# Kernel tuning notes

Measured on AMD Instinct MI355X. Metric: run time of the kernel, lower is better.

Reference implementation:

```python
import jax, jax.numpy as jnp
import numpy as np

N = 100000
E = 3200000
D_IN = 128
HEADS = 4
OUT_CH = 64


def setup_inputs() -> dict:
    key = jax.random.key(0)
    kx, ke, kw, kb = jax.random.split(key, 4)
    x = jax.random.normal(kx, (N, D_IN), dtype=jnp.float32)
    edge_index = jax.random.randint(ke, (2, E), 0, N, dtype=jnp.int64)
    # nn.Linear(in_channels, out_channels*heads): weight [out, in] in torch; store as [in, out] for x @ W
    W = jax.random.normal(kw, (D_IN, OUT_CH * HEADS), dtype=jnp.float32) * (1.0 / np.sqrt(D_IN))
    b = jax.random.normal(kb, (OUT_CH * HEADS,), dtype=jnp.float32) * 0.01
    return {"x": x, "edge_index": edge_index, "W": W, "b": b}


def reference(x, edge_index, W, b):
    src, dst = edge_index[0], edge_index[1]
    n = x.shape[0]
    # scatter-add of gathered src features into dst rows (segment sum)
    agg = jax.ops.segment_sum(x[src], dst, num_segments=n)  # [N, D_IN]
    count = jax.ops.segment_sum(jnp.ones((src.shape[0], 1), x.dtype), dst, num_segments=n)  # [N, 1]
    agg = agg / (count + 1e-8)
    # linear on (x + agg); view to [N, heads*out_channels] is a no-op reshape
    return (x + agg) @ W + b
```

## Files before the change

kernel.cpp:

```cpp
#include <hip/hip_runtime.h>

#define N_NODES 100000
#define D_IN 128
#define D_OUT 256
#define NBLK 256
#define NBKT 256
#define BSH  9
#define BNODES 512
#define NBUCKETS ((N_NODES + BNODES - 1) / BNODES)
#define CAP  19456
#define CAPC 12544

typedef __attribute__((ext_vector_type(8))) short short8_t;
typedef __attribute__((ext_vector_type(4))) float f32x4;

__device__ inline unsigned short f2bf_rne(float f) {
    unsigned u = __float_as_uint(f);
    u += 0x7fffu + ((u >> 16) & 1u);
    return (unsigned short)(u >> 16);
}

__global__ __launch_bounds__(256) void convert_kernel(
    const float* __restrict__ x, ushort* __restrict__ xb, int n4)
{
    int i = blockIdx.x * 256 + threadIdx.x;
    if (i < n4) {
        float4 v = ((const float4*)x)[i];
        ushort4 r;
        r.x = f2bf_rne(v.x); r.y = f2bf_rne(v.y);
        r.z = f2bf_rne(v.z); r.w = f2bf_rne(v.w);
        ((ushort4*)xb)[i] = r;
    }
}

__global__ __launch_bounds__(256) void wfrag_kernel(
    const float* __restrict__ W, short8_t* __restrict__ wfrag)
{
    int tid  = blockIdx.x * 256 + threadIdx.x;
    int lane = tid & 63;
    int fi   = tid >> 6;
    int ks   = fi >> 4, nt = fi & 15;
    int k0   = ks * 32 + (lane >> 4) * 8;
    int col  = nt * 16 + (lane & 15);
    short8_t v;
    #pragma unroll
    for (int e = 0; e < 8; e++)
        v[e] = (short)f2bf_rne(W[(size_t)(k0 + e) * D_OUT + col]);
    wfrag[tid] = v;
}

__global__ __launch_bounds__(256) void binA_hist(
    const int* __restrict__ dst, int* __restrict__ blockHist, int E, int chunk)
{
    __shared__ int h[NBKT];
    int b = blockIdx.x, t = threadIdx.x;
    h[t] = 0;
    __syncthreads();
    int e0 = b * chunk, e1 = min(e0 + chunk, E);
    for (int e = e0 + t; e < e1; e += 256)
        atomicAdd(&h[dst[e] >> BSH], 1);
    __syncthreads();
    blockHist[b * NBKT + t] = h[t];
}

__global__ __launch_bounds__(256) void binA_scan(
    int* __restrict__ blockHist, int* __restrict__ bucketTotal)
{
    __shared__ int wsum[4];
    int bucket = blockIdx.x;
    int t = threadIdx.x, lane = t & 63, w = t >> 6;
    int v = blockHist[t * NBKT + bucket];
    int s = v;
    #pragma unroll
    for (int d = 1; d < 64; d <<= 1) {
        int u = __shfl_up(s, d);
        if (lane >= d) s += u;
    }
    if (lane == 63) wsum[w] = s;
    __syncthreads();
    int wo = 0;
    for (int j = 0; j < w; j++) wo += wsum[j];
    blockHist[t * NBKT + bucket] = wo + s - v;
    if (t == 255) {
        int tot = 0;
        for (int j = 0; j < 4; j++) tot += wsum[j];
        bucketTotal[bucket] = tot;
    }
}

__global__ __launch_bounds__(256) void binA_scanbase(
    const int* __restrict__ bucketTotal, int* __restrict__ bucketBase)
{
    __shared__ int wsum[4];
    int t = threadIdx.x, lane = t & 63, w = t >> 6;
    int v = bucketTotal[t];
    int s = v;
    #pragma unroll
    for (int d = 1; d < 64; d <<= 1) {
        int u = __shfl_up(s, d);
        if (lane >= d) s += u;
    }
    if (lane == 63) wsum[w] = s;
    __syncthreads();
    int wo = 0;
    for (int j = 0; j < w; j++) wo += wsum[j];
    bucketBase[t] = wo + s - v;
}

__global__ __launch_bounds__(256) void binA_scatter(
    const int* __restrict__ src, const int* __restrict__ dst,
    const int* __restrict__ blockHist, const int* __restrict__ bucketBase,
    unsigned* __restrict__ pairs, int E, int chunk)
{
    __shared__ unsigned stage[CAPC];
    __shared__ int cnt[NBKT];
    __shared__ int lofs[NBKT];
    __shared__ int rankl[NBKT];
    __shared__ int gcur[NBKT];
    __shared__ int wsum[4];

    int b = blockIdx.x, t = threadIdx.x, lane = t & 63, w = t >> 6;
    int e0 = b * chunk, e1 = min(e0 + chunk, E);

    gcur[t] = bucketBase[t] + blockHist[b * NBKT + t];
    __syncthreads();

    for (int c0 = e0; c0 < e1; c0 += CAPC) {
        int c1 = c0 + CAPC; if (c1 > e1) c1 = e1;

        cnt[t] = 0;
        __syncthreads();

        for (int e = c0 + t; e < c1; e += 256)
            atomicAdd(&cnt[dst[e] >> BSH], 1);
        __syncthreads();

        {
            int v = cnt[t];
            int s = v;
            #pragma unroll
            for (int d = 1; d < 64; d <<= 1) {
                int u = __shfl_up(s, d);
                if (lane >= d) s += u;
            }
            if (lane == 63) wsum[w] = s;
            __syncthreads();
            int wo = 0;
            for (int j = 0; j < w; j++) wo += wsum[j];
            int excl = wo + s - v;
            lofs[t]  = excl;
            rankl[t] = excl;
        }
        __syncthreads();

        for (int e = c0 + t; e < c1; e += 256) {
            int d = dst[e];
            int bin = d >> BSH;
            int pos = atomicAdd(&rankl[bin], 1);
            stage[pos] = ((unsigned)(d & (BNODES - 1)) << 17) | (unsigned)src[e];
        }
        __syncthreads();

        for (int bin = w; bin < NBKT; bin += 4) {
            int lo = lofs[bin], c = cnt[bin], g = gcur[bin];
            for (int i = lane; i < c; i += 64)
                pairs[g + i] = stage[lo + i];
        }
        __syncthreads();

        gcur[t] += cnt[t];
        __syncthreads();
    }
}

__global__ __launch_bounds__(256) void binB_sort(
    unsigned* __restrict__ pairs, const int* __restrict__ bucketBase,
    int* __restrict__ offs_g, int* __restrict__ deg_g)
{
    __shared__ unsigned stage[CAP];
    __shared__ int hist[BNODES];
    __shared__ int rank[BNODES];
    __shared__ int wsum[4];

    int b = blockIdx.x, t = threadIdx.x, lane = t & 63, w = t >> 6;
    int e0 = bucketBase[b], e1 = bucketBase[b + 1];
    int cnt = e1 - e0;
    if (cnt > CAP) cnt = CAP;

    hist[t] = 0; hist[t + 256] = 0;
    __syncthreads();

    for (int i = t; i < cnt; i += 256) {
        unsigned p = pairs[e0 + i];
        stage[i] = p;
        atomicAdd(&hist[p >> 17], 1);
    }
    __syncthreads();

    int a0 = hist[t * 2], a1 = hist[t * 2 + 1];
    int v = a0 + a1;
    int s = v;
    #pragma unroll
    for (int d = 1; d < 64; d <<= 1) {
        int u = __shfl_up(s, d);
        if (lane >= d) s += u;
    }
    if (lane == 63) wsum[w] = s;
    __syncthreads();
    int wo = 0;
    for (int j = 0; j < w; j++) wo += wsum[j];
    int excl = wo + s - v;

    rank[t * 2]     = excl;
    rank[t * 2 + 1] = excl + a0;
    int node = (b << BSH) + t * 2;
    if (node < N_NODES) {
        offs_g[node] = e0 + excl;
        deg_g[node]  = a0;
    }
    if (node + 1 < N_NODES) {
        offs_g[node + 1] = e0 + excl + a0;
        deg_g[node + 1]  = a1;
    }
    __syncthreads();

    for (int i = t; i < cnt; i += 256) {
        unsigned p = stage[i];
        int pos = atomicAdd(&rank[p >> 17], 1);
        pairs[e0 + pos] = p & 0x1FFFFu;
    }
}

template <bool USE_BF16>
__global__ __launch_bounds__(256) void fused_kernel(
    const float* __restrict__ x,
    const ushort* __restrict__ xb,
    const int* __restrict__ offs,
    const int* __restrict__ deg,
    const int* __restrict__ sorted_src,
    const short8_t* __restrict__ wfrag,
    const float* __restrict__ b,
    float* __restrict__ out)
{
    __shared__ __align__(16) ushort shb[16 * D_IN];

    int n0   = blockIdx.x * 16;
    int t    = threadIdx.x;
    int lane = t & 63;
    int w    = t >> 6;

    for (int nn = 0; nn < 4; nn++) {
        int nl = w * 4 + nn;
        int n  = n0 + nl;
        int start = offs[n];
        int d     = deg[n];
        float accx = 0.0f, accy = 0.0f;
        for (int base = 0; base < d; base += 64) {
            int m = d - base; if (m > 64) m = 64;
            int id = (lane < m) ? sorted_src[start + base + lane] : 0;
            int j = 0;
            for (; j + 4 <= m; j += 4) {
                int s0 = __builtin_amdgcn_readlane(id, j);
                int s1 = __builtin_amdgcn_readlane(id, j + 1);
                int s2 = __builtin_amdgcn_readlane(id, j + 2);
                int s3 = __builtin_amdgcn_readlane(id, j + 3);
                if (USE_BF16) {
                    ushort2 u0 = ((const ushort2*)(xb + (size_t)s0 * D_IN))[lane];
                    ushort2 u1 = ((const ushort2*)(xb + (size_t)s1 * D_IN))[lane];
                    ushort2 u2 = ((const ushort2*)(xb + (size_t)s2 * D_IN))[lane];
                    ushort2 u3 = ((const ushort2*)(xb + (size_t)s3 * D_IN))[lane];
                    accx += __uint_as_float((unsigned)u0.x << 16)
                          + __uint_as_float((unsigned)u1.x << 16)
                          + __uint_as_float((unsigned)u2.x << 16)
                          + __uint_as_float((unsigned)u3.x << 16);
                    accy += __uint_as_float((unsigned)u0.y << 16)
                          + __uint_as_float((unsigned)u1.y << 16)
                          + __uint_as_float((unsigned)u2.y << 16)
                          + __uint_as_float((unsigned)u3.y << 16);
                } else {
                    float2 v0 = ((const float2*)(x + (size_t)s0 * D_IN))[lane];
                    float2 v1 = ((const float2*)(x + (size_t)s1 * D_IN))[lane];
                    float2 v2 = ((const float2*)(x + (size_t)s2 * D_IN))[lane];
                    float2 v3 = ((const float2*)(x + (size_t)s3 * D_IN))[lane];
                    accx += v0.x + v1.x + v2.x + v3.x;
                    accy += v0.y + v1.y + v2.y + v3.y;
                }
            }
            for (; j < m; j++) {
                int s0 = __builtin_amdgcn_readlane(id, j);
                if (USE_BF16) {
                    ushort2 u0 = ((const ushort2*)(xb + (size_t)s0 * D_IN))[lane];
                    accx += __uint_as_float((unsigned)u0.x << 16);
                    accy += __uint_as_float((unsigned)u0.y << 16);
                } else {
                    float2 v0 = ((const float2*)(x + (size_t)s0 * D_IN))[lane];
                    accx += v0.x; accy += v0.y;
                }
            }
        }
        float invc = 1.0f / ((float)d + 1e-8f);
        float2 xv = ((const float2*)(x + (size_t)n * D_IN))[lane];
        float hx = xv.x + accx * invc;
        float hy = xv.y + accy * invc;
        unsigned hp = ((unsigned)f2bf_rne(hy) << 16) | (unsigned)f2bf_rne(hx);
        unsigned byteoff = ((unsigned)(nl * 256 + lane * 4)) ^ (((unsigned)nl & 7u) << 4);
        *(unsigned*)((char*)shb + byteoff) = hp;
    }
    __syncthreads();

    const int r  = lane & 15;
    const int hi = lane >> 4;

    short8_t afrag[4];
    #pragma unroll
    for (int ks = 0; ks < 4; ks++) {
        unsigned aoff = ((unsigned)(r * 256 + ks * 64 + hi * 16)) ^ (((unsigned)r & 7u) << 4);
        afrag[ks] = *(const short8_t*)((const char*)shb + aoff);
    }

    f32x4 zero = {0.0f, 0.0f, 0.0f, 0.0f};
    f32x4 acc0 = zero, acc1 = zero, acc2 = zero, acc3 = zero;
    const int nt0 = w * 4;
    #pragma unroll
    for (int ks = 0; ks < 4; ks++) {
        short8_t b0 = wfrag[(ks * 16 + nt0    ) * 64 + lane];
        short8_t b1 = wfrag[(ks * 16 + nt0 + 1) * 64 + lane];
        short8_t b2 = wfrag[(ks * 16 + nt0 + 2) * 64 + lane];
        short8_t b3 = wfrag[(ks * 16 + nt0 + 3) * 64 + lane];
        acc0 = __builtin_amdgcn_mfma_f32_16x16x32_bf16(afrag[ks], b0, acc0, 0, 0, 0);
        acc1 = __builtin_amdgcn_mfma_f32_16x16x32_bf16(afrag[ks], b1, acc1, 0, 0, 0);
        acc2 = __builtin_amdgcn_mfma_f32_16x16x32_bf16(afrag[ks], b2, acc2, 0, 0, 0);
        acc3 = __builtin_amdgcn_mfma_f32_16x16x32_bf16(afrag[ks], b3, acc3, 0, 0, 0);
    }

    #pragma unroll
    for (int nt = 0; nt < 4; nt++) {
        f32x4 a = (nt == 0) ? acc0 : (nt == 1) ? acc1 : (nt == 2) ? acc2 : acc3;
        int col = (nt0 + nt) * 16 + r;
        float bias = b[col];
        #pragma unroll
        for (int reg = 0; reg < 4; reg++) {
            int node = n0 + hi * 4 + reg;
            out[(size_t)node * D_OUT + col] = a[reg] + bias;
        }
    }
}

extern "C" void kernel_launch(void* const* d_in, const int* in_sizes, int n_in,
                              void* d_out, int out_size, void* d_ws, size_t ws_size,
                              hipStream_t stream)
{
    const float* x  = (const float*)d_in[0];
    const int*   ei = (const int*)d_in[1];
    const float* W  = (const float*)d_in[2];
    const float* b  = (const float*)d_in[3];
    float*       out = (float*)d_out;

    const int E = in_sizes[1] / 2;
    const int* src = ei;
    const int* dst = ei + E;
    const int chunk = (E + NBLK - 1) / NBLK;

    const size_t xb_bytes   = (size_t)N_NODES * D_IN * 2;
    const size_t pairs_b    = (size_t)E * 4;
    const size_t bh_b       = (size_t)NBLK * NBKT * 4;
    const size_t small_b    = (size_t)NBKT * 4;
    const size_t nodes_b    = (size_t)N_NODES * 4;
    const size_t wf_b       = (size_t)4096 * 16;
    const size_t need_bf16  = xb_bytes + pairs_b + bh_b + 2 * small_b
                            + 2 * nodes_b + wf_b;
    const bool use_bf16 = (ws_size >= need_bf16);

    char* p = (char*)d_ws;
    ushort* xb = nullptr;
    if (use_bf16) { xb = (ushort*)p; p += xb_bytes; }
    unsigned* pairs  = (unsigned*)p;  p += pairs_b;
    int* blockHist   = (int*)p;       p += bh_b;
    int* bucketTotal = (int*)p;       p += small_b;
    int* bucketBase  = (int*)p;       p += small_b;
    int* offs        = (int*)p;       p += nodes_b;
    int* deg         = (int*)p;       p += nodes_b;
    short8_t* wfrag  = (short8_t*)p;

    if (use_bf16) {
        int n4 = N_NODES * D_IN / 4;
        convert_kernel<<<dim3((n4 + 255) / 256), dim3(256), 0, stream>>>(x, xb, n4);
    }
    wfrag_kernel<<<dim3(16), dim3(256), 0, stream>>>(W, wfrag);

    binA_hist    <<<dim3(NBLK), dim3(256), 0, stream>>>(dst, blockHist, E, chunk);
    binA_scan    <<<dim3(NBKT), dim3(256), 0, stream>>>(blockHist, bucketTotal);
    binA_scanbase<<<dim3(1),    dim3(256), 0, stream>>>(bucketTotal, bucketBase);
    binA_scatter <<<dim3(NBLK), dim3(256), 0, stream>>>(
        src, dst, blockHist, bucketBase, pairs, E, chunk);
    binB_sort    <<<dim3(NBUCKETS), dim3(256), 0, stream>>>(
        pairs, bucketBase, offs, deg);

    if (use_bf16)
        fused_kernel<true><<<dim3(N_NODES / 16), dim3(256), 0, stream>>>(
            x, xb, offs, deg, (const int*)pairs, wfrag, b, out);
    else
        fused_kernel<false><<<dim3(N_NODES / 16), dim3(256), 0, stream>>>(
            x, xb, offs, deg, (const int*)pairs, wfrag, b, out);
}
```

Before: 415.4 us.

## Merge preprocessing kernels, fold bucket scan into consumers, widen blocks to 1024

```diff
diff --git a/kernel.cpp b/kernel.cpp
--- a/kernel.cpp
+++ b/kernel.cpp
@@ -10,6 +10,10 @@
 #define NBUCKETS ((N_NODES + BNODES - 1) / BNODES)
 #define CAP  19456
 #define CAPC 12544
+#define N4   (N_NODES * D_IN / 4)
+#define CONV_BLKS ((N4 + 4095) / 4096)
+#define WF_BLK0 (NBLK + CONV_BLKS)
+#define K1_GRID (WF_BLK0 + 4)
 
 typedef __attribute__((ext_vector_type(8))) short short8_t;
 typedef __attribute__((ext_vector_type(4))) float f32x4;
@@ -20,47 +24,52 @@
     return (unsigned short)(u >> 16);
 }
 
-__global__ __launch_bounds__(256) void convert_kernel(
-    const float* __restrict__ x, ushort* __restrict__ xb, int n4)
-{
-    int i = blockIdx.x * 256 + threadIdx.x;
-    if (i < n4) {
-        float4 v = ((const float4*)x)[i];
-        ushort4 r;
-        r.x = f2bf_rne(v.x); r.y = f2bf_rne(v.y);
-        r.z = f2bf_rne(v.z); r.w = f2bf_rne(v.w);
-        ((ushort4*)xb)[i] = r;
-    }
-}
-
-__global__ __launch_bounds__(256) void wfrag_kernel(
-    const float* __restrict__ W, short8_t* __restrict__ wfrag)
-{
-    int tid  = blockIdx.x * 256 + threadIdx.x;
-    int lane = tid & 63;
-    int fi   = tid >> 6;
-    int ks   = fi >> 4, nt = fi & 15;
-    int k0   = ks * 32 + (lane >> 4) * 8;
-    int col  = nt * 16 + (lane & 15);
-    short8_t v;
-    #pragma unroll
-    for (int e = 0; e < 8; e++)
-        v[e] = (short)f2bf_rne(W[(size_t)(k0 + e) * D_OUT + col]);
-    wfrag[tid] = v;
-}
-
-__global__ __launch_bounds__(256) void binA_hist(
-    const int* __restrict__ dst, int* __restrict__ blockHist, int E, int chunk)
+__global__ __launch_bounds__(1024) void pre_kernel(
+    const float* __restrict__ x, ushort* __restrict__ xb,
+    const float* __restrict__ W, short8_t* __restrict__ wfrag,
+    const int* __restrict__ dst, int* __restrict__ blockHist,
+    int E, int chunk, int do_conv)
 {
     __shared__ int h[NBKT];
-    int b = blockIdx.x, t = threadIdx.x;
-    h[t] = 0;
-    __syncthreads();
-    int e0 = b * chunk, e1 = min(e0 + chunk, E);
-    for (int e = e0 + t; e < e1; e += 256)
-        atomicAdd(&h[dst[e] >> BSH], 1);
-    __syncthreads();
-    blockHist[b * NBKT + t] = h[t];
+    int bid = blockIdx.x, t = threadIdx.x;
+
+    if (bid < NBLK) {
+        if (t < NBKT) h[t] = 0;
+        __syncthreads();
+        int e0 = bid * chunk, e1 = min(e0 + chunk, E);
+        for (int e = e0 + t; e < e1; e += 1024)
+            atomicAdd(&h[dst[e] >> BSH], 1);
+        __syncthreads();
+        if (t < NBKT) blockHist[bid * NBKT + t] = h[t];
+    } else if (bid < WF_BLK0) {
+        if (!do_conv) return;
+        int base = (bid - NBLK) * 4096 + t;
+        #pragma unroll
+        for (int k = 0; k < 4; k++) {
+            int i = base + k * 1024;
+            if (i < N4) {
+                float4 v = ((const float4*)x)[i];
+                ushort4 r;
+                r.x = f2bf_rne(v.x); r.y = f2bf_rne(v.y);
+                r.z = f2bf_rne(v.z); r.w = f2bf_rne(v.w);
+                ((ushort4*)xb)[i] = r;
+            }
+        }
+    } else {
+        int tid = (bid - WF_BLK0) * 1024 + t;
+        if (tid < 4096) {
+            int lane = tid & 63;
+            int fi   = tid >> 6;
+            int ks = fi >> 4, nt = fi & 15;
+            int k0 = ks * 32 + (lane >> 4) * 8;
+            int col = nt * 16 + (lane & 15);
+            short8_t v;
+            #pragma unroll
+            for (int e = 0; e < 8; e++)
+                v[e] = (short)f2bf_rne(W[(size_t)(k0 + e) * D_OUT + col]);
+            wfrag[tid] = v;
+        }
+    }
 }
 
 __global__ __launch_bounds__(256) void binA_scan(
@@ -88,72 +97,67 @@
     }
 }
 
-__global__ __launch_bounds__(256) void binA_scanbase(
-    const int* __restrict__ bucketTotal, int* __restrict__ bucketBase)
-{
-    __shared__ int wsum[4];
-    int t = threadIdx.x, lane = t & 63, w = t >> 6;
-    int v = bucketTotal[t];
-    int s = v;
-    #pragma unroll
-    for (int d = 1; d < 64; d <<= 1) {
-        int u = __shfl_up(s, d);
-        if (lane >= d) s += u;
-    }
-    if (lane == 63) wsum[w] = s;
-    __syncthreads();
-    int wo = 0;
-    for (int j = 0; j < w; j++) wo += wsum[j];
-    bucketBase[t] = wo + s - v;
-}
-
-__global__ __launch_bounds__(256) void binA_scatter(
+__global__ __launch_bounds__(1024) void binA_scatter(
     const int* __restrict__ src, const int* __restrict__ dst,
-    const int* __restrict__ blockHist, const int* __restrict__ bucketBase,
+    const int* __restrict__ blockHist, const int* __restrict__ bucketTotal,
     unsigned* __restrict__ pairs, int E, int chunk)
 {
     __shared__ unsigned stage[CAPC];
-    __shared__ int cnt[NBKT];
-    __shared__ int lofs[NBKT];
-    __shared__ int rankl[NBKT];
-    __shared__ int gcur[NBKT];
-    __shared__ int wsum[4];
+    __shared__ int cnt[NBKT], lofs[NBKT], rankl[NBKT], gcur[NBKT];
+    __shared__ int wsum[16];
 
     int b = blockIdx.x, t = threadIdx.x, lane = t & 63, w = t >> 6;
     int e0 = b * chunk, e1 = min(e0 + chunk, E);
 
-    gcur[t] = bucketBase[t] + blockHist[b * NBKT + t];
+    int sv = 0, ss = 0;
+    if (t < NBKT) {
+        sv = bucketTotal[t]; ss = sv;
+        #pragma unroll
+        for (int d = 1; d < 64; d <<= 1) {
+            int u = __shfl_up(ss, d);
+            if (lane >= d) ss += u;
+        }
+        if (lane == 63) wsum[w] = ss;
+    }
+    __syncthreads();
+    if (t < NBKT) {
+        int wo = 0;
+        for (int j = 0; j < w; j++) wo += wsum[j];
+        gcur[t] = (wo + ss - sv) + blockHist[b * NBKT + t];
+    }
     __syncthreads();
 
     for (int c0 = e0; c0 < e1; c0 += CAPC) {
         int c1 = c0 + CAPC; if (c1 > e1) c1 = e1;
 
-        cnt[t] = 0;
-        __syncthreads();
-
-        for (int e = c0 + t; e < c1; e += 256)
+        if (t < NBKT) cnt[t] = 0;
+        __syncthreads();
+
+        for (int e = c0 + t; e < c1; e += 1024)
             atomicAdd(&cnt[dst[e] >> BSH], 1);
         __syncthreads();
 
-        {
-            int v = cnt[t];
-            int s = v;
+        int v2 = 0, s2 = 0;
+        if (t < NBKT) {
+            v2 = cnt[t]; s2 = v2;
             #pragma unroll
             for (int d = 1; d < 64; d <<= 1) {
-                int u = __shfl_up(s, d);
-                if (lane >= d) s += u;
+                int u = __shfl_up(s2, d);
+                if (lane >= d) s2 += u;
             }
-            if (lane == 63) wsum[w] = s;
-            __syncthreads();
+            if (lane == 63) wsum[w] = s2;
+        }
+        __syncthreads();
+        if (t < NBKT) {
             int wo = 0;
             for (int j = 0; j < w; j++) wo += wsum[j];
-            int excl = wo + s - v;
+            int excl = wo + s2 - v2;
             lofs[t]  = excl;
             rankl[t] = excl;
         }
         __syncthreads();
 
-        for (int e = c0 + t; e < c1; e += 256) {
+        for (int e = c0 + t; e < c1; e += 1024) {
             int d = dst[e];
             int bin = d >> BSH;
             int pos = atomicAdd(&rankl[bin], 1);
@@ -161,70 +165,86 @@
         }
         __syncthreads();
 
-        for (int bin = w; bin < NBKT; bin += 4) {
+        for (int bin = w; bin < NBKT; bin += 16) {
             int lo = lofs[bin], c = cnt[bin], g = gcur[bin];
             for (int i = lane; i < c; i += 64)
                 pairs[g + i] = stage[lo + i];
         }
         __syncthreads();
 
-        gcur[t] += cnt[t];
-        __syncthreads();
-    }
-}
-
-__global__ __launch_bounds__(256) void binB_sort(
-    unsigned* __restrict__ pairs, const int* __restrict__ bucketBase,
+        if (t < NBKT) gcur[t] += cnt[t];
+        __syncthreads();
+    }
+}
+
+__global__ __launch_bounds__(1024) void binB_sort(
+    unsigned* __restrict__ pairs, const int* __restrict__ bucketTotal,
     int* __restrict__ offs_g, int* __restrict__ deg_g)
 {
     __shared__ unsigned stage[CAP];
     __shared__ int hist[BNODES];
     __shared__ int rank[BNODES];
-    __shared__ int wsum[4];
+    __shared__ int wsum[16];
+    __shared__ int ebase[2];
 
     int b = blockIdx.x, t = threadIdx.x, lane = t & 63, w = t >> 6;
-    int e0 = bucketBase[b], e1 = bucketBase[b + 1];
-    int cnt = e1 - e0;
+
+    int sv = 0, ss = 0;
+    if (t < NBKT) {
+        sv = bucketTotal[t]; ss = sv;
+        #pragma unroll
+        for (int d = 1; d < 64; d <<= 1) {
+            int u = __shfl_up(ss, d);
+            if (lane >= d) ss += u;
+        }
+        if (lane == 63) wsum[w] = ss;
+    }
+    __syncthreads();
+    if (t < NBKT) {
+        int wo = 0;
+        for (int j = 0; j < w; j++) wo += wsum[j];
+        if (t == b) { ebase[0] = wo + ss - sv; ebase[1] = sv; }
+    }
+    __syncthreads();
+    const int e0 = ebase[0];
+    int cnt = ebase[1];
     if (cnt > CAP) cnt = CAP;
 
-    hist[t] = 0; hist[t + 256] = 0;
-    __syncthreads();
-
-    for (int i = t; i < cnt; i += 256) {
+    if (t < BNODES) hist[t] = 0;
+    __syncthreads();
+
+    for (int i = t; i < cnt; i += 1024) {
         unsigned p = pairs[e0 + i];
         stage[i] = p;
         atomicAdd(&hist[p >> 17], 1);
     }
     __syncthreads();
 
-    int a0 = hist[t * 2], a1 = hist[t * 2 + 1];
-    int v = a0 + a1;
-    int s = v;
-    #pragma unroll
-    for (int d = 1; d < 64; d <<= 1) {
-        int u = __shfl_up(s, d);
-        if (lane >= d) s += u;
-    }
-    if (lane == 63) wsum[w] = s;
-    __syncthreads();
-    int wo = 0;
-    for (int j = 0; j < w; j++) wo += wsum[j];
-    int excl = wo + s - v;
-
-    rank[t * 2]     = excl;
-    rank[t * 2 + 1] = excl + a0;
-    int node = (b << BSH) + t * 2;
-    if (node < N_NODES) {
-        offs_g[node] = e0 + excl;
-        deg_g[node]  = a0;
-    }
-    if (node + 1 < N_NODES) {
-        offs_g[node + 1] = e0 + excl + a0;
-        deg_g[node + 1]  = a1;
-    }
-    __syncthreads();
-
-    for (int i = t; i < cnt; i += 256) {
+    int v2 = 0, s2 = 0;
+    if (t < BNODES) {
+        v2 = hist[t]; s2 = v2;
+        #pragma unroll
+        for (int d = 1; d < 64; d <<= 1) {
+            int u = __shfl_up(s2, d);
+            if (lane >= d) s2 += u;
+        }
+        if (lane == 63) wsum[w] = s2;
+    }
+    __syncthreads();
+    if (t < BNODES) {
+        int wo = 0;
+        for (int j = 0; j < w; j++) wo += wsum[j];
+        int excl = wo + s2 - v2;
+        rank[t] = excl;
+        int node = (b << BSH) + t;
+        if (node < N_NODES) {
+            offs_g[node] = e0 + excl;
+            deg_g[node]  = v2;
+        }
+    }
+    __syncthreads();
+
+    for (int i = t; i < cnt; i += 1024) {
         unsigned p = stage[i];
         int pos = atomicAdd(&rank[p >> 17], 1);
         pairs[e0 + pos] = p & 0x1FFFFu;
@@ -367,7 +387,7 @@
     const size_t small_b    = (size_t)NBKT * 4;
     const size_t nodes_b    = (size_t)N_NODES * 4;
     const size_t wf_b       = (size_t)4096 * 16;
-    const size_t need_bf16  = xb_bytes + pairs_b + bh_b + 2 * small_b
+    const size_t need_bf16  = xb_bytes + pairs_b + bh_b + small_b
                             + 2 * nodes_b + wf_b;
     const bool use_bf16 = (ws_size >= need_bf16);
 
@@ -377,24 +397,17 @@
     unsigned* pairs  = (unsigned*)p;  p += pairs_b;
     int* blockHist   = (int*)p;       p += bh_b;
     int* bucketTotal = (int*)p;       p += small_b;
-    int* bucketBase  = (int*)p;       p += small_b;
     int* offs        = (int*)p;       p += nodes_b;
     int* deg         = (int*)p;       p += nodes_b;
     short8_t* wfrag  = (short8_t*)p;
 
-    if (use_bf16) {
-        int n4 = N_NODES * D_IN / 4;
-        convert_kernel<<<dim3((n4 + 255) / 256), dim3(256), 0, stream>>>(x, xb, n4);
-    }
-    wfrag_kernel<<<dim3(16), dim3(256), 0, stream>>>(W, wfrag);
-
-    binA_hist    <<<dim3(NBLK), dim3(256), 0, stream>>>(dst, blockHist, E, chunk);
-    binA_scan    <<<dim3(NBKT), dim3(256), 0, stream>>>(blockHist, bucketTotal);
-    binA_scanbase<<<dim3(1),    dim3(256), 0, stream>>>(bucketTotal, bucketBase);
-    binA_scatter <<<dim3(NBLK), dim3(256), 0, stream>>>(
-        src, dst, blockHist, bucketBase, pairs, E, chunk);
-    binB_sort    <<<dim3(NBUCKETS), dim3(256), 0, stream>>>(
-        pairs, bucketBase, offs, deg);
+    pre_kernel  <<<dim3(K1_GRID), dim3(1024), 0, stream>>>(
+        x, xb, W, wfrag, dst, blockHist, E, chunk, use_bf16 ? 1 : 0);
+    binA_scan   <<<dim3(NBKT), dim3(256), 0, stream>>>(blockHist, bucketTotal);
+    binA_scatter<<<dim3(NBLK), dim3(1024), 0, stream>>>(
+        src, dst, blockHist, bucketTotal, pairs, E, chunk);
+    binB_sort   <<<dim3(NBUCKETS), dim3(1024), 0, stream>>>(
+        pairs, bucketTotal, offs, deg);
 
     if (use_bf16)
         fused_kernel<true><<<dim3(N_NODES / 16), dim3(256), 0, stream>>>(
```

After: 350.1 us. 1.19x faster.
